# Kernel optimization log

Hardware: AMD Instinct MI355X
Metric: run time of the kernel (lower is better)

## Reference

```python
import jax, jax.numpy as jnp
import numpy as np

N = 50000      # nodes
E = 800000     # edges (avg degree 16)
IN = 128       # in_channels
OUT = 2        # out_channels
HID = 100 * OUT  # MAX_CHANNELS * out_channels = 200
MSG_EPS = 1e-7   # GENConv message eps
BN_EPS = 1e-5    # BatchNorm1d eps


def _gen_conv(x, src, dst, w1, b1, g, be, w2, b2):
    """PyG GENConv with defaults: aggr='softmax', t=1.0, msg_norm=False,
    MLP=[c, 2c, c_out] with BatchNorm1d+ReLU between layers (train-mode BN)."""
    # message: relu(x_j) + eps  -> [E, d]
    msg = jnp.maximum(x[src], 0.0) + MSG_EPS
    # scatter softmax over incoming edges of each destination node (t=1)
    m = jax.ops.segment_max(msg, dst, num_segments=N)          # [N, d]
    m = jnp.where(jnp.isfinite(m), m, 0.0)                      # isolated nodes
    ex = jnp.exp(msg - m[dst])                                  # [E, d]
    s = jax.ops.segment_sum(ex, dst, num_segments=N)            # [N, d]
    alpha = ex / (s[dst] + 1e-16)                               # [E, d]
    out = jax.ops.segment_sum(msg * alpha, dst, num_segments=N) # [N, d]
    out = out + x                                               # residual with x_dst
    # MLP: Linear -> BatchNorm(batch stats) -> ReLU -> Linear
    h = out @ w1 + b1                                           # [N, 2d]
    mu = h.mean(axis=0)
    var = h.var(axis=0)
    h = (h - mu) * jax.lax.rsqrt(var + BN_EPS) * g + be
    h = jnp.maximum(h, 0.0)
    return h @ w2 + b2


def setup_inputs() -> dict:
    key = jax.random.key(0)
    ks = jax.random.split(key, 8)
    rn = lambda k, shp, s: jax.random.normal(k, shp, jnp.float32) * s
    mid1, mid2 = 2 * IN, 2 * HID
    return {
        "x": rn(ks[0], (N, IN), 1.0),
        "edge_index": jax.random.randint(ks[1], (2, E), 0, N, jnp.int32),
        "c1_w1": rn(ks[2], (IN, mid1), 0.05), "c1_b1": jnp.zeros((mid1,), jnp.float32),
        "c1_g": jnp.ones((mid1,), jnp.float32), "c1_beta": jnp.zeros((mid1,), jnp.float32),
        "c1_w2": rn(ks[3], (mid1, HID), 0.05), "c1_b2": jnp.zeros((HID,), jnp.float32),
        "c2_w1": rn(ks[4], (HID, mid2), 0.05), "c2_b1": jnp.zeros((mid2,), jnp.float32),
        "c2_g": jnp.ones((mid2,), jnp.float32), "c2_beta": jnp.zeros((mid2,), jnp.float32),
        "c2_w2": rn(ks[5], (mid2, OUT), 0.05), "c2_b2": jnp.zeros((OUT,), jnp.float32),
    }


def reference(x, edge_index, c1_w1, c1_b1, c1_g, c1_beta, c1_w2, c1_b2,
              c2_w1, c2_b1, c2_g, c2_beta, c2_w2, c2_b2):
    src, dst = edge_index[0], edge_index[1]
    h = jnp.maximum(_gen_conv(x, src, dst, c1_w1, c1_b1, c1_g, c1_beta, c1_w2, c1_b2), 0.0)
    # Dropout(p=0.1) is identity in eval mode (deterministic reference)
    return jnp.maximum(_gen_conv(h, src, dst, c2_w1, c2_b1, c2_g, c2_beta, c2_w2, c2_b2), 0.0)
```

## Files before the change

kernel.cpp:

```cpp
#include <hip/hip_runtime.h>
#include <hip/hip_bf16.h>
#include <stdint.h>

#define NNODES 50000
#define NEDGES 800000
#define DIN 128
#define DHID 200
#define MID1 256
#define MID2 400
#define NBB ((NNODES + 127) / 128)
#define LOG2E 1.4426950408889634f
#define LN2 0.6931471805599453f
#define GK_SPLIT 112
#define GCH 208
#define GNP 40
#define NBUCK 98
#define BCAP 16384
#define EPB 4096
#define BIN_NB ((NEDGES + EPB - 1) / EPB)
#define PREP_NB ((NNODES * DIN / 4 + 255) / 256)

typedef __hip_bfloat16 bf16;
typedef __attribute__((ext_vector_type(8))) short short8;
typedef __attribute__((ext_vector_type(4))) float floatx4;
typedef unsigned short ushort;

__device__ __forceinline__ float b2f(bf16 v) { return __bfloat162float(v); }
__device__ __forceinline__ bf16 f2b(float v) { return __float2bfloat16(v); }
__device__ __forceinline__ float bits2f(ushort b) {
    unsigned u = ((unsigned)b) << 16;
    return __uint_as_float(u);
}
__device__ __forceinline__ ushort f2bits(float f) {
    bf16 h = __float2bfloat16(f);
    return *(ushort*)&h;
}
__device__ __forceinline__ float ldin(const void* p, size_t i, int f32) {
    return f32 ? ((const float*)p)[i] : __bfloat162float(((const bf16*)p)[i]);
}
__device__ __forceinline__ void ldin4(const void* p, size_t i, int f32, float* v) {
    if (f32) {
        float4 f = *(const float4*)((const float*)p + i);
        v[0] = f.x; v[1] = f.y; v[2] = f.z; v[3] = f.w;
    } else {
        ushort4 u = *(const ushort4*)((const bf16*)p + i);
        v[0] = bits2f(u.x); v[1] = bits2f(u.y); v[2] = bits2f(u.z); v[3] = bits2f(u.w);
    }
}
__device__ __forceinline__ float fexp2(float x) {
#if __has_builtin(__builtin_amdgcn_exp2f)
    return __builtin_amdgcn_exp2f(x);
#else
    return exp2f(x);
#endif
}
__device__ __forceinline__ floatx4 mfma16(short8 a, short8 b, floatx4 c) {
    return __builtin_amdgcn_mfma_f32_16x16x32_bf16(a, b, c, 0, 0, 0);
}
__device__ __forceinline__ void acc4(ushort4 u, float* s, float* p) {
    ushort uu[4];
    *(ushort4*)uu = u;
#pragma unroll
    for (int c = 0; c < 4; c++) {
        float v = bits2f(uu[c]);
        float ee = fexp2(v);
        s[c] += ee;
        p[c] = fmaf(v, ee, p[c]);
    }
}
__device__ __forceinline__ void acc2(ushort2 u, float* s, float* p) {
    float v0 = bits2f(u.x), v1 = bits2f(u.y);
    float e0 = fexp2(v0), e1 = fexp2(v1);
    s[0] += e0;
    p[0] = fmaf(v0, e0, p[0]);
    s[1] += e1;
    p[1] = fmaf(v1, e1, p[1]);
}

#define TW (DIN * MID1 + MID1 * DHID + DHID * MID2)
__global__ __launch_bounds__(256) void binprep_kernel(const int* __restrict__ src,
                                                      const int* __restrict__ dst,
                                                      const void* __restrict__ g,
                                                      int* __restrict__ flag,
                                                      unsigned* __restrict__ bbuf,
                                                      int* __restrict__ gcur,
                                                      const void* __restrict__ W1, bf16* __restrict__ Wt1,
                                                      const void* __restrict__ W2, bf16* __restrict__ Wt2,
                                                      const void* __restrict__ W3, bf16* __restrict__ Wt3,
                                                      const void* __restrict__ X, bf16* __restrict__ M1,
                                                      ushort* __restrict__ dummy) {
    __shared__ int cnt[NBUCK], cur[NBUCK];
    int tid = threadIdx.x;
    int bx = blockIdx.x;
    if (bx < BIN_NB) {
        if (bx == 0 && tid == 0)
            *flag = (((const unsigned*)g)[0] == 0x3F800000u) ? 1 : 0;
        if (tid < NBUCK) cnt[tid] = 0;
        __syncthreads();
        int e0 = bx * EPB;
        unsigned pk[16];
        int bk[16];
#pragma unroll
        for (int i = 0; i < 16; i++) {
            int e = e0 + i * 256 + tid;
            if (e < NEDGES) {
                int d = dst[e], s = src[e];
                pk[i] = ((unsigned)d << 16) | (unsigned)s;
                bk[i] = d >> 9;
                atomicAdd(&cnt[bk[i]], 1);
            } else {
                bk[i] = -1;
            }
        }
        __syncthreads();
        if (tid < NBUCK) cur[tid] = atomicAdd(&gcur[tid], cnt[tid]);
        __syncthreads();
#pragma unroll
        for (int i = 0; i < 16; i++) {
            if (bk[i] >= 0) {
                int off = atomicAdd(&cur[bk[i]], 1);
                bbuf[(size_t)bk[i] * BCAP + off] = pk[i];
            }
        }
    } else {
        int f32 = (((const unsigned*)g)[0] == 0x3F800000u) ? 1 : 0;
        int idx = (bx - BIN_NB) * 256 + tid;
        const int S1 = DIN * MID1, S2 = MID1 * DHID;
        if (idx < TW) {
            const void* W;
            bf16* Wt;
            int K, N, li;
            if (idx < S1) { W = W1; Wt = Wt1; K = DIN; N = MID1; li = idx; }
            else if (idx < S1 + S2) { W = W2; Wt = Wt2; K = MID1; N = DHID; li = idx - S1; }
            else { W = W3; Wt = Wt3; K = DHID; N = MID2; li = idx - S1 - S2; }
            int k = li / N, n = li - k * N;
            Wt[(size_t)n * K + k] = f2b(ldin(W, li, f32));
        }
        if (idx < DHID) dummy[idx] = 0xC300;
        int i = idx * 4;
        if (i < NNODES * DIN) {
            float v[4];
            ldin4(X, i, f32, v);
            ushort4 o;
            o.x = f2bits((fmaxf(v[0], 0.f) + 1e-7f) * LOG2E);
            o.y = f2bits((fmaxf(v[1], 0.f) + 1e-7f) * LOG2E);
            o.z = f2bits((fmaxf(v[2], 0.f) + 1e-7f) * LOG2E);
            o.w = f2bits((fmaxf(v[3], 0.f) + 1e-7f) * LOG2E);
            *(ushort4*)(M1 + i) = o;
        }
    }
}

__global__ __launch_bounds__(512) void histscanA_kernel(const unsigned* __restrict__ bbuf,
                                                        const int* __restrict__ gcur,
                                                        int* __restrict__ rowptr,
                                                        int* __restrict__ blocksums) {
    __shared__ int hc[512];
    int b = blockIdx.x, t = threadIdx.x;
    int base = b << 9;
    int nn = min(512, NNODES - base);
    hc[t] = 0;
    __syncthreads();
    int cnt = gcur[b];
    const unsigned* eb = bbuf + (size_t)b * BCAP;
    for (int i = t; i < cnt; i += 512) atomicAdd(&hc[(eb[i] >> 16) - base], 1);
    __syncthreads();
    int v = hc[t];
#pragma unroll
    for (int off = 1; off < 512; off <<= 1) {
        int o = (t >= off) ? hc[t - off] : 0;
        __syncthreads();
        hc[t] += o;
        __syncthreads();
    }
    if (t < nn) rowptr[base + t] = hc[t] - v;
    if (t == 511) blocksums[b] = hc[511];
}

__global__ __launch_bounds__(512) void scanscatter_kernel(const unsigned* __restrict__ bbuf,
                                                          const int* __restrict__ gcur,
                                                          const int* __restrict__ blocksums,
                                                          int* __restrict__ rowptr,
                                                          int* __restrict__ ssrc) {
    __shared__ int sh[128];
    __shared__ int lc[512];
    int b = blockIdx.x, t = threadIdx.x;
    int base = b << 9;
    int nn = min(512, NNODES - base);
    if (t < 128) sh[t] = (t < NBUCK) ? blocksums[t] : 0;
    __syncthreads();
#pragma unroll
    for (int off = 1; off < 128; off <<= 1) {
        int o = (t < 128 && t >= off) ? sh[t - off] : 0;
        __syncthreads();
        if (t < 128) sh[t] += o;
        __syncthreads();
    }
    int boff = (b > 0) ? sh[b - 1] : 0;
    if (t < nn) {
        int r = rowptr[base + t] + boff;
        rowptr[base + t] = r;
        lc[t] = r;
    }
    if (b == NBUCK - 1 && t == 0) rowptr[NNODES] = NEDGES;
    __syncthreads();
    int cnt = gcur[b];
    const unsigned* eb = bbuf + (size_t)b * BCAP;
    for (int i = t; i < cnt; i += 512) {
        unsigned p = eb[i];
        int node = (int)(p >> 16) - base;
        int idx = atomicAdd(&lc[node], 1);
        ssrc[idx] = (int)(p & 0xFFFFu);
    }
}

__global__ __launch_bounds__(256) void agg1_kernel(const void* __restrict__ X,
                                                   const bf16* __restrict__ M1,
                                                   const int* __restrict__ rowptr,
                                                   const int* __restrict__ ssrc,
                                                   const ushort* __restrict__ dummy,
                                                   const int* __restrict__ flag,
                                                   bf16* __restrict__ out) {
    int f32 = *flag;
    int lane = threadIdx.x & 63;
    int n = blockIdx.x * 4 + (threadIdx.x >> 6);
    int r0 = __builtin_amdgcn_readfirstlane(rowptr[n]);
    int deg = __builtin_amdgcn_readfirstlane(rowptr[n + 1]) - r0;
    int boff = lane << 2;
    const char* M1b = (const char*)M1;
    const char* dp = (const char*)dummy;
    float s[2] = {0.f, 0.f}, p[2] = {0.f, 0.f};
    int nfull = deg >> 3;
    for (int b = 0; b < nfull; b++) {
        const int* ep = ssrc + r0 + (b << 3);
        ushort2 u[8];
#pragma unroll
        for (int k = 0; k < 8; k++)
            u[k] = *(const ushort2*)(M1b + ((size_t)(unsigned)ep[k] << 8) + boff);
#pragma unroll
        for (int k = 0; k < 8; k++) acc2(u[k], s, p);
    }
    int rem = deg & 7;
    if (rem) {
        const int* ep = ssrc + r0 + (nfull << 3);
        ushort2 u[8];
#pragma unroll
        for (int k = 0; k < 8; k++) {
            const char* rp = (k < rem) ? (M1b + ((size_t)(unsigned)ep[k] << 8)) : dp;
            u[k] = *(const ushort2*)(rp + boff);
        }
#pragma unroll
        for (int k = 0; k < 8; k++) acc2(u[k], s, p);
    }
    int c0 = lane * 2;
    float xc0 = ldin(X, (size_t)n * DIN + c0, f32);
    float xc1 = ldin(X, (size_t)n * DIN + c0 + 1, f32);
    ushort2 o;
    o.x = f2bits(fmaf(LN2, p[0] / (s[0] + 1e-16f), xc0));
    o.y = f2bits(fmaf(LN2, p[1] / (s[1] + 1e-16f), xc1));
    *(ushort2*)(out + (size_t)n * DIN + c0) = o;
}

__global__ __launch_bounds__(256) void agg2_kernel(const bf16* __restrict__ M2,
                                                   const int* __restrict__ rowptr,
                                                   const int* __restrict__ ssrc,
                                                   const ushort* __restrict__ dummy,
                                                   bf16* __restrict__ out) {
    int lane = threadIdx.x & 63;
    int n = blockIdx.x * 4 + (threadIdx.x >> 6);
    int r0 = __builtin_amdgcn_readfirstlane(rowptr[n]);
    int deg = __builtin_amdgcn_readfirstlane(rowptr[n + 1]) - r0;
    bool act = lane < 50;
    int boff = (act ? lane : 49) << 3;
    const char* M2b = (const char*)M2;
    const char* dp = (const char*)dummy;
    float s[4] = {0.f, 0.f, 0.f, 0.f}, p[4] = {0.f, 0.f, 0.f, 0.f};
    int nfull = deg >> 3;
    for (int b = 0; b < nfull; b++) {
        const int* ep = ssrc + r0 + (b << 3);
        ushort4 u[8];
#pragma unroll
        for (int k = 0; k < 8; k++)
            u[k] = *(const ushort4*)(M2b + (size_t)((unsigned)ep[k] * 400u) + boff);
#pragma unroll
        for (int k = 0; k < 8; k++) acc4(u[k], s, p);
    }
    int rem = deg & 7;
    if (rem) {
        const int* ep = ssrc + r0 + (nfull << 3);
        ushort4 u[8];
#pragma unroll
        for (int k = 0; k < 8; k++) {
            const char* rp = (k < rem) ? (M2b + (size_t)((unsigned)ep[k] * 400u)) : dp;
            u[k] = *(const ushort4*)(rp + boff);
        }
#pragma unroll
        for (int k = 0; k < 8; k++) acc4(u[k], s, p);
    }
    if (act) {
        ushort4 u = *(const ushort4*)(M2b + (size_t)n * 400 + boff);
        float vn[4] = {bits2f(u.x), bits2f(u.y), bits2f(u.z), bits2f(u.w)};
        ushort4 o;
        o.x = f2bits(LN2 * (p[0] / (s[0] + 1e-16f) + vn[0]) - 1e-7f);
        o.y = f2bits(LN2 * (p[1] / (s[1] + 1e-16f) + vn[1]) - 1e-7f);
        o.z = f2bits(LN2 * (p[2] / (s[2] + 1e-16f) + vn[2]) - 1e-7f);
        o.w = f2bits(LN2 * (p[3] / (s[3] + 1e-16f) + vn[3]) - 1e-7f);
        *(ushort4*)(out + (size_t)n * DHID + 4 * lane) = o;
    }
}

template <int MODE, int NT, int KK, int NCOL>
__global__ __launch_bounds__(512, 4) void bgemm(const bf16* __restrict__ A,
                                                const bf16* __restrict__ Bt,
                                                const void* __restrict__ bias,
                                                const int* __restrict__ flag,
                                                const float* __restrict__ sc,
                                                const float* __restrict__ offs,
                                                float* __restrict__ bnsum,
                                                float* __restrict__ bnsumsq,
                                                const void* __restrict__ gam,
                                                const void* __restrict__ bet,
                                                const void* __restrict__ w2,
                                                bf16* __restrict__ Out, int ostride,
                                                float* __restrict__ fscr, int M) {
    constexpr int KP = (KK + 31) & ~31;
    constexpr int KS = KP / 32;
    constexpr int KV8 = KP / 8;
    __shared__ short Bs[NT * 16][KP + 8];
    __shared__ float scs[MODE == 1 ? KK : 1];
    __shared__ float ofs[MODE == 1 ? KK : 1];
    int f32 = *flag;
    int tid = threadIdx.x;
    int cb = blockIdx.y * NCOL;

    if (MODE == 1) {
        for (int c = tid; c < KK; c += 512) {
            float mu = bnsum[c] / (float)NNODES;
            float var = fmaxf(bnsumsq[c] / (float)NNODES - mu * mu, 0.f);
            float rstd = rsqrtf(var + 1e-5f);
            float sv = rstd * ldin(gam, c, f32);
            scs[c] = sv;
            ofs[c] = ldin(bet, c, f32) - mu * sv;
        }
    }
    for (int idx = tid; idx < NT * 16 * KV8; idx += 512) {
        int col = idx / KV8, kq = (idx - col * KV8) * 8;
        uint4 v = {0, 0, 0, 0};
        if (col < NCOL && kq < KK) v = *(const uint4*)(Bt + (size_t)(cb + col) * KK + kq);
        *(uint4*)&Bs[col][kq] = v;
    }
    __syncthreads();

    int w = tid >> 6, L = tid & 63;
    int lm = L & 15, q = L >> 4;
    int rw = blockIdx.x * 128 + w * 16;
    int ar = rw + lm;
    bool rok = ar < M;

    uint4 af[KS];
#pragma unroll
    for (int s = 0; s < KS; s++) {
        int k = s * 32 + q * 8;
        af[s] = (uint4){0, 0, 0, 0};
        if (rok && k + 8 <= KK) af[s] = *(const uint4*)(A + (size_t)ar * KK + k);
    }

    floatx4 acc[NT];
#pragma unroll
    for (int t = 0; t < NT; t++) acc[t] = (floatx4){0.f, 0.f, 0.f, 0.f};

#pragma unroll
    for (int s = 0; s < KS; s++) {
        short8 as;
        if (MODE == 1) {
            int ch = s * 32 + q * 8;
            ushort us[8];
            *(uint4*)us = af[s];
#pragma unroll
            for (int j = 0; j < 8; j++)
                us[j] = f2bits(fmaxf(fmaf(bits2f(us[j]), scs[ch + j], ofs[ch + j]), 0.f));
            as = *(short8*)us;
        } else {
            as = *(short8*)&af[s];
        }
#pragma unroll
        for (int t = 0; t < NT; t++) {
            short8 bf = *(const short8*)&Bs[t * 16 + lm][s * 32 + q * 8];
            acc[t] = mfma16(as, bf, acc[t]);
        }
    }

    if (MODE == 0) {
        float* fs = (float*)&Bs[0][0];
        float* fq = fs + 8 * 256;
        __syncthreads();
#pragma unroll
        for (int t = 0; t < NT; t++) {
            int col = t * 16 + lm;
            float bb = ldin(bias, col, f32);
            float cs = 0.f, cq = 0.f;
#pragma unroll
            for (int r = 0; r < 4; r++) {
                int gm = rw + q * 4 + r;
                if (gm < M) {
                    float v = acc[t][r] + bb;
                    Out[(size_t)gm * ostride + col] = f2b(v);
                    cs += v;
                    cq += v * v;
                }
            }
            cs += __shfl_xor(cs, 16, 64); cq += __shfl_xor(cq, 16, 64);
            cs += __shfl_xor(cs, 32, 64); cq += __shfl_xor(cq, 32, 64);
            if (q == 0) {
                fs[w * 256 + col] = cs;
                fq[w * 256 + col] = cq;
            }
        }
        __syncthreads();
        for (int c = tid; c < NT * 16; c += 512) {
            float ts = 0.f, tq = 0.f;
#pragma unroll
            for (int ww = 0; ww < 8; ww++) {
                ts += fs[ww * 256 + c];
                tq += fq[ww * 256 + c];
            }
            atomicAdd(&bnsum[c], ts);
            atomicAdd(&bnsumsq[c], tq);
        }
    }
    if (MODE == 1) {
#pragma unroll
        for (int t = 0; t < NT; t++) {
            int col = t * 16 + lm;
            if (col < NCOL) {
                int gg = cb + col;
                float bb = ldin(bias, gg, f32);
#pragma unroll
                for (int r = 0; r < 4; r++) {
                    int gm = rw + q * 4 + r;
                    if (gm < M) {
                        float v = acc[t][r] + bb;
                        Out[(size_t)gm * ostride + gg] = f2b((fmaxf(v, 0.f) + 1e-7f) * LOG2E);
                    }
                }
            }
        }
    }
    if (MODE == 2) {
        float s0[4] = {0.f, 0.f, 0.f, 0.f}, s1[4] = {0.f, 0.f, 0.f, 0.f};
#pragma unroll
        for (int t = 0; t < NT; t++) {
            int col = t * 16 + lm;
            if (col < NCOL) {
                int gg = cb + col;
                float bb = ldin(bias, gg, f32);
                float scv = sc[gg], ofv = offs[gg];
                float w20 = ldin(w2, 2 * gg, f32), w21 = ldin(w2, 2 * gg + 1, f32);
#pragma unroll
                for (int r = 0; r < 4; r++) {
                    float vn = fmaxf((acc[t][r] + bb) * scv + ofv, 0.f);
                    s0[r] = fmaf(vn, w20, s0[r]);
                    s1[r] = fmaf(vn, w21, s1[r]);
                }
            }
        }
#pragma unroll
        for (int d = 1; d < 16; d <<= 1) {
#pragma unroll
            for (int r = 0; r < 4; r++) {
                s0[r] += __shfl_xor(s0[r], d, 64);
                s1[r] += __shfl_xor(s1[r], d, 64);
            }
        }
        if (lm == 0) {
#pragma unroll
            for (int r = 0; r < 4; r++) {
                int gm = rw + q * 4 + r;
                if (gm < M) {
                    fscr[(size_t)gm * 8 + blockIdx.y * 2 + 0] = s0[r];
                    fscr[(size_t)gm * 8 + blockIdx.y * 2 + 1] = s1[r];
                }
            }
        }
    }
}

__global__ __launch_bounds__(512) void gram_kernel(const bf16* __restrict__ X,
                                                   float* __restrict__ pg) {
    __shared__ short T[GCH][GNP];
    int tid = threadIdx.x;
    int w = tid >> 6, L = tid & 63;
    int lm = L & 15, q = L >> 4;
    floatx4 acc[2][13];
#pragma unroll
    for (int c = 0; c < 2; c++)
#pragma unroll
        for (int t = 0; t < 13; t++) acc[c][t] = (floatx4){0.f, 0.f, 0.f, 0.f};

    const int chunks = (NNODES + 32 * GK_SPLIT - 1) / (32 * GK_SPLIT);
    int base0 = blockIdx.x * chunks * 32;
    for (int ch = 0; ch < chunks; ch++) {
        int nb = base0 + ch * 32;
#pragma unroll
        for (int p = 0; p < 4; p++) {
            int idx = tid + p * 512;
            if (idx < 1600) {
                int nl = idx & 31, cq = idx >> 5;
                int gn = nb + nl;
                ushort4 u = {0, 0, 0, 0};
                if (gn < NNODES) u = *(const ushort4*)(X + (size_t)gn * DHID + cq * 4);
                T[cq * 4 + 0][nl] = (short)u.x;
                T[cq * 4 + 1][nl] = (short)u.y;
                T[cq * 4 + 2][nl] = (short)u.z;
                T[cq * 4 + 3][nl] = (short)u.w;
            }
        }
        if (tid < 256) {
            int nl = tid & 31, c = 200 + (tid >> 5);
            int gn = nb + nl;
            T[c][nl] = (c == 200 && gn < NNODES) ? (short)0x3F80 : (short)0;
        }
        __syncthreads();
        short8 af[13];
#pragma unroll
        for (int t = 0; t < 13; t++) af[t] = *(const short8*)&T[t * 16 + lm][q * 8];
#pragma unroll
        for (int c = 0; c < 2; c++) {
            int cj = w + c * 8;
            if (cj < 13) {
                short8 bf = *(const short8*)&T[cj * 16 + lm][q * 8];
#pragma unroll
                for (int t = 0; t < 13; t++) acc[c][t] = mfma16(af[t], bf, acc[c][t]);
            }
        }
        __syncthreads();
    }
    float* pgb = pg + (size_t)blockIdx.x * (GCH * GCH);
#pragma unroll
    for (int c = 0; c < 2; c++) {
        int cj = w + c * 8;
        if (cj < 13) {
#pragma unroll
            for (int t = 0; t < 13; t++)
#pragma unroll
                for (int r = 0; r < 4; r++)
                    pgb[(size_t)(t * 16 + q * 4 + r) * GCH + cj * 16 + lm] = acc[c][t][r];
        }
    }
}

__global__ void greduce_kernel(const float* __restrict__ pg, float* __restrict__ G) {
    int e = blockIdx.x * 256 + threadIdx.x;
    if (e < GCH * GCH) {
        float s = 0.f;
        for (int b = 0; b < GK_SPLIT; b++) s += pg[(size_t)b * (GCH * GCH) + e];
        G[e] = s;
    }
}

__global__ __launch_bounds__(256) void bn2_finish(const float* __restrict__ G,
                                                  const bf16* __restrict__ Wt3,
                                                  const void* __restrict__ b1,
                                                  const void* __restrict__ g,
                                                  const void* __restrict__ be,
                                                  const int* __restrict__ flag,
                                                  float* __restrict__ sc,
                                                  float* __restrict__ off) {
    __shared__ float wl[200];
    __shared__ float red[256];
    __shared__ float dsh;
    int f32 = *flag;
    int c = blockIdx.x;
    int t = threadIdx.x;
    if (t < 200) wl[t] = b2f(Wt3[(size_t)c * DHID + t]);
    __syncthreads();
    float di = 0.f;
    if (t <= 200) {
        const float* Gr = G + (size_t)t * GCH;
        for (int j = 0; j < 200; j++) di = fmaf(Gr[j], wl[j], di);
    }
    red[t] = (t < 200) ? wl[t] * di : 0.f;
    if (t == 200) dsh = di;
    __syncthreads();
    for (int o = 128; o > 0; o >>= 1) {
        if (t < o) red[t] += red[t + o];
        __syncthreads();
    }
    if (t == 0) {
        float d = dsh;
        float bc = ldin(b1, c, f32);
        float mu = d / (float)NNODES + bc;
        float eh2 = (red[0] + 2.f * bc * d) / (float)NNODES + bc * bc;
        float var = fmaxf(eh2 - mu * mu, 0.f);
        float rstd = rsqrtf(var + 1e-5f);
        float s = rstd * ldin(g, c, f32);
        sc[c] = s;
        off[c] = ldin(be, c, f32) - mu * s;
    }
}

__global__ void final_combine(const float* __restrict__ fscr, const void* __restrict__ b2,
                              const int* __restrict__ flag, void* __restrict__ outp, int M) {
    int f32 = *flag;
    int n = blockIdx.x * 256 + threadIdx.x;
    if (n < M) {
        const float* f = fscr + (size_t)n * 8;
        float v0 = fmaxf(f[0] + f[2] + f[4] + f[6] + ldin(b2, 0, f32), 0.f);
        float v1 = fmaxf(f[1] + f[3] + f[5] + f[7] + ldin(b2, 1, f32), 0.f);
        if (f32) {
            ((float*)outp)[2 * n] = v0;
            ((float*)outp)[2 * n + 1] = v1;
        } else {
            ((bf16*)outp)[2 * n] = f2b(v0);
            ((bf16*)outp)[2 * n + 1] = f2b(v1);
        }
    }
}

extern "C" void kernel_launch(void* const* d_in, const int* in_sizes, int n_in,
                              void* d_out, int out_size, void* d_ws, size_t ws_size,
                              hipStream_t stream) {
    const void* x = d_in[0];
    const int* ei = (const int*)d_in[1];
    const void* c1_w1 = d_in[2];
    const void* c1_b1 = d_in[3];
    const void* c1_g = d_in[4];
    const void* c1_be = d_in[5];
    const void* c1_w2 = d_in[6];
    const void* c1_b2 = d_in[7];
    const void* c2_w1 = d_in[8];
    const void* c2_b1 = d_in[9];
    const void* c2_g = d_in[10];
    const void* c2_be = d_in[11];
    const void* c2_w2 = d_in[12];
    const void* c2_b2 = d_in[13];

    const int* src = ei;
    const int* dst = ei + NEDGES;

    uint8_t* w = (uint8_t*)d_ws;
    int* rowptr = (int*)(w + 0);
    bf16* wT1 = (bf16*)(w + 204800);
    bf16* wT2 = (bf16*)(w + 270336);
    bf16* wT3 = (bf16*)(w + 409600);
    int* ssrc = (int*)(w + 614400);
    float* bnbuf = (float*)(w + 3814400);
    float* sum1 = bnbuf, *sumsq1 = bnbuf + 256;
    int* gcur = (int*)(bnbuf + 512);
    float* sc2 = bnbuf + 1824, *off2 = bnbuf + 2224;
    int* flag_in = (int*)(bnbuf + 2624);
    int* blocksums = (int*)(bnbuf + 2640);
    ushort* dummyrow = (ushort*)(bnbuf + 2840);
    uint8_t* bufA = w + 3830784;
    uint8_t* bufB = w + 23830784;
    unsigned* bbuf = (unsigned*)bufA;
    bf16* out1 = (bf16*)bufA;
    bf16* h1 = (bf16*)bufA;
    float* pg = (float*)bufA;
    float* Gm = (float*)(bufA + 19400000);
    float* fscr = (float*)bufA;
    bf16* M1 = (bf16*)bufB;
    bf16* t1 = (bf16*)bufB;
    bf16* out2 = (bf16*)bufB;

    hipMemsetAsync(bnbuf, 0, 1312 * sizeof(float), stream);

    binprep_kernel<<<BIN_NB + PREP_NB, 256, 0, stream>>>(
        src, dst, c1_g, flag_in, bbuf, gcur,
        c1_w1, wT1, c1_w2, wT2, c2_w1, wT3, x, M1, dummyrow);
    histscanA_kernel<<<NBUCK, 512, 0, stream>>>(bbuf, gcur, rowptr, blocksums);
    scanscatter_kernel<<<NBUCK, 512, 0, stream>>>(bbuf, gcur, blocksums, rowptr, ssrc);

    agg1_kernel<<<NNODES / 4, 256, 0, stream>>>(x, M1, rowptr, ssrc, dummyrow, flag_in,
                                                out1);
    bgemm<0, 16, 128, 256><<<dim3(NBB, 1), 512, 0, stream>>>(
        out1, wT1, c1_b1, flag_in, nullptr, nullptr,
        sum1, sumsq1, nullptr, nullptr, nullptr,
        t1, MID1, nullptr, NNODES);
    bgemm<1, 7, 256, 100><<<dim3(NBB, 2), 512, 0, stream>>>(
        t1, wT2, c1_b2, flag_in, nullptr, nullptr,
        sum1, sumsq1, c1_g, c1_be, nullptr,
        h1, DHID, nullptr, NNODES);

    agg2_kernel<<<NNODES / 4, 256, 0, stream>>>(h1, rowptr, ssrc, dummyrow, out2);
    gram_kernel<<<GK_SPLIT, 512, 0, stream>>>(out2, pg);
    greduce_kernel<<<(GCH * GCH + 255) / 256, 256, 0, stream>>>(pg, Gm);
    bn2_finish<<<MID2, 256, 0, stream>>>(Gm, wT3, c2_b1, c2_g, c2_be, flag_in, sc2, off2);
    bgemm<2, 7, 200, 100><<<dim3(NBB, 4), 512, 0, stream>>>(
        out2, wT3, c2_b1, flag_in, sc2, off2,
        nullptr, nullptr, nullptr, nullptr, c2_w2,
        nullptr, 0, fscr, NNODES);
    final_combine<<<(NNODES + 255) / 256, 256, 0, stream>>>(fscr, c2_b2, flag_in,
                                                            d_out, NNODES);
}
```

Baseline: 337.2 us.

## Merge CSR scan kernels and replace gram partial reduction with atomics

Fuses the histogram/scan and scan/scatter kernels into one CSR kernel that computes the bucket offset prefix directly from per-bucket counts, dropping a launch and the blocksums round trip. The gram kernel now accumulates its partial results straight into the global Gram matrix with float atomicAdd instead of writing 112 partial matrices and reducing them in a separate kernel. The Gram buffer is zeroed by extra blocks appended to the agg2 launch. This removes two launches and a large partial-sum write and read, at the cost of atomic contention on the Gram matrix and a summation order that is no longer deterministic.

```diff
diff --git a/kernel.cpp b/kernel.cpp
--- a/kernel.cpp
+++ b/kernel.cpp
@@ -14,6 +14,7 @@
 #define GK_SPLIT 112
 #define GCH 208
 #define GNP 40
+#define GZB 64
 #define NBUCK 98
 #define BCAP 16384
 #define EPB 4096
@@ -151,14 +152,26 @@
     }
 }
 
-__global__ __launch_bounds__(512) void histscanA_kernel(const unsigned* __restrict__ bbuf,
-                                                        const int* __restrict__ gcur,
-                                                        int* __restrict__ rowptr,
-                                                        int* __restrict__ blocksums) {
+__global__ __launch_bounds__(512) void csr_kernel(const unsigned* __restrict__ bbuf,
+                                                  const int* __restrict__ gcur,
+                                                  int* __restrict__ rowptr,
+                                                  int* __restrict__ ssrc) {
+    __shared__ int pre[128];
     __shared__ int hc[512];
+    __shared__ int lc[512];
     int b = blockIdx.x, t = threadIdx.x;
     int base = b << 9;
     int nn = min(512, NNODES - base);
+    if (t < 128) pre[t] = (t < NBUCK) ? gcur[t] : 0;
+    __syncthreads();
+#pragma unroll
+    for (int off = 1; off < 128; off <<= 1) {
+        int o = (t < 128 && t >= off) ? pre[t - off] : 0;
+        __syncthreads();
+        if (t < 128) pre[t] += o;
+        __syncthreads();
+    }
+    int boff = (b > 0) ? pre[b - 1] : 0;
     hc[t] = 0;
     __syncthreads();
     int cnt = gcur[b];
@@ -173,39 +186,11 @@
         hc[t] += o;
         __syncthreads();
     }
-    if (t < nn) rowptr[base + t] = hc[t] - v;
-    if (t == 511) blocksums[b] = hc[511];
-}
-
-__global__ __launch_bounds__(512) void scanscatter_kernel(const unsigned* __restrict__ bbuf,
-                                                          const int* __restrict__ gcur,
-                                                          const int* __restrict__ blocksums,
-                                                          int* __restrict__ rowptr,
-                                                          int* __restrict__ ssrc) {
-    __shared__ int sh[128];
-    __shared__ int lc[512];
-    int b = blockIdx.x, t = threadIdx.x;
-    int base = b << 9;
-    int nn = min(512, NNODES - base);
-    if (t < 128) sh[t] = (t < NBUCK) ? blocksums[t] : 0;
-    __syncthreads();
-#pragma unroll
-    for (int off = 1; off < 128; off <<= 1) {
-        int o = (t < 128 && t >= off) ? sh[t - off] : 0;
-        __syncthreads();
-        if (t < 128) sh[t] += o;
-        __syncthreads();
-    }
-    int boff = (b > 0) ? sh[b - 1] : 0;
-    if (t < nn) {
-        int r = rowptr[base + t] + boff;
-        rowptr[base + t] = r;
-        lc[t] = r;
-    }
+    int r = hc[t] - v + boff;
+    if (t < nn) rowptr[base + t] = r;
+    lc[t] = r;
     if (b == NBUCK - 1 && t == 0) rowptr[NNODES] = NEDGES;
     __syncthreads();
-    int cnt = gcur[b];
-    const unsigned* eb = bbuf + (size_t)b * BCAP;
     for (int i = t; i < cnt; i += 512) {
         unsigned p = eb[i];
         int node = (int)(p >> 16) - base;
@@ -265,9 +250,16 @@
                                                    const int* __restrict__ rowptr,
                                                    const int* __restrict__ ssrc,
                                                    const ushort* __restrict__ dummy,
+                                                   float* __restrict__ Gm,
                                                    bf16* __restrict__ out) {
+    int bx = blockIdx.x;
+    if (bx >= NNODES / 4) {
+        int z = (bx - NNODES / 4) * 256 + threadIdx.x;
+        for (int e = z; e < GCH * GCH; e += GZB * 256) Gm[e] = 0.f;
+        return;
+    }
     int lane = threadIdx.x & 63;
-    int n = blockIdx.x * 4 + (threadIdx.x >> 6);
+    int n = bx * 4 + (threadIdx.x >> 6);
     int r0 = __builtin_amdgcn_readfirstlane(rowptr[n]);
     int deg = __builtin_amdgcn_readfirstlane(rowptr[n + 1]) - r0;
     bool act = lane < 50;
@@ -486,7 +478,7 @@
 }
 
 __global__ __launch_bounds__(512) void gram_kernel(const bf16* __restrict__ X,
-                                                   float* __restrict__ pg) {
+                                                   float* __restrict__ Gm) {
     __shared__ short T[GCH][GNP];
     int tid = threadIdx.x;
     int w = tid >> 6, L = tid & 63;
@@ -535,7 +527,6 @@
         }
         __syncthreads();
     }
-    float* pgb = pg + (size_t)blockIdx.x * (GCH * GCH);
 #pragma unroll
     for (int c = 0; c < 2; c++) {
         int cj = w + c * 8;
@@ -544,17 +535,9 @@
             for (int t = 0; t < 13; t++)
 #pragma unroll
                 for (int r = 0; r < 4; r++)
-                    pgb[(size_t)(t * 16 + q * 4 + r) * GCH + cj * 16 + lm] = acc[c][t][r];
-        }
-    }
-}
-
-__global__ void greduce_kernel(const float* __restrict__ pg, float* __restrict__ G) {
-    int e = blockIdx.x * 256 + threadIdx.x;
-    if (e < GCH * GCH) {
-        float s = 0.f;
-        for (int b = 0; b < GK_SPLIT; b++) s += pg[(size_t)b * (GCH * GCH) + e];
-        G[e] = s;
+                    atomicAdd(&Gm[(size_t)(t * 16 + q * 4 + r) * GCH + cj * 16 + lm],
+                              acc[c][t][r]);
+        }
     }
 }
 
@@ -649,27 +632,24 @@
     int* gcur = (int*)(bnbuf + 512);
     float* sc2 = bnbuf + 1824, *off2 = bnbuf + 2224;
     int* flag_in = (int*)(bnbuf + 2624);
-    int* blocksums = (int*)(bnbuf + 2640);
     ushort* dummyrow = (ushort*)(bnbuf + 2840);
     uint8_t* bufA = w + 3830784;
     uint8_t* bufB = w + 23830784;
     unsigned* bbuf = (unsigned*)bufA;
     bf16* out1 = (bf16*)bufA;
     bf16* h1 = (bf16*)bufA;
-    float* pg = (float*)bufA;
-    float* Gm = (float*)(bufA + 19400000);
     float* fscr = (float*)bufA;
     bf16* M1 = (bf16*)bufB;
     bf16* t1 = (bf16*)bufB;
     bf16* out2 = (bf16*)bufB;
+    float* Gm = (float*)(bufB + 20000000);
 
     hipMemsetAsync(bnbuf, 0, 1312 * sizeof(float), stream);
 
     binprep_kernel<<<BIN_NB + PREP_NB, 256, 0, stream>>>(
         src, dst, c1_g, flag_in, bbuf, gcur,
         c1_w1, wT1, c1_w2, wT2, c2_w1, wT3, x, M1, dummyrow);
-    histscanA_kernel<<<NBUCK, 512, 0, stream>>>(bbuf, gcur, rowptr, blocksums);
-    scanscatter_kernel<<<NBUCK, 512, 0, stream>>>(bbuf, gcur, blocksums, rowptr, ssrc);
+    csr_kernel<<<NBUCK, 512, 0, stream>>>(bbuf, gcur, rowptr, ssrc);
 
     agg1_kernel<<<NNODES / 4, 256, 0, stream>>>(x, M1, rowptr, ssrc, dummyrow, flag_in,
                                                 out1);
@@ -682,9 +662,9 @@
         sum1, sumsq1, c1_g, c1_be, nullptr,
         h1, DHID, nullptr, NNODES);
 
-    agg2_kernel<<<NNODES / 4, 256, 0, stream>>>(h1, rowptr, ssrc, dummyrow, out2);
-    gram_kernel<<<GK_SPLIT, 512, 0, stream>>>(out2, pg);
-    greduce_kernel<<<(GCH * GCH + 255) / 256, 256, 0, stream>>>(pg, Gm);
+    agg2_kernel<<<NNODES / 4 + GZB, 256, 0, stream>>>(h1, rowptr, ssrc, dummyrow, Gm,
+                                                      out2);
+    gram_kernel<<<GK_SPLIT, 512, 0, stream>>>(out2, Gm);
     bn2_finish<<<MID2, 256, 0, stream>>>(Gm, wT3, c2_b1, c2_g, c2_be, flag_in, sc2, off2);
     bgemm<2, 7, 200, 100><<<dim3(NBB, 4), 512, 0, stream>>>(
         out2, wT3, c2_b1, flag_in, sc2, off2,
```

Result: slower. 354.5 us (+5.1%).
